# Kernel tuning notes

Hardware: AMD Instinct MI355X
Metric: run time of the kernel (lower is better)

## Reference

```python
import math
import jax, jax.numpy as jnp
import numpy as np

B, S, D, H = 4, 2048, 1024, 16
HD = D // H
EPS = 1e-5
NEG = 1e10


def setup_inputs() -> dict:
    key = jax.random.key(0)
    ks = jax.random.split(key, 6)
    std = 0.02
    return {
        "x": jax.random.normal(ks[0], (B, S, D), dtype=jnp.float32),
        "ln1_w": jnp.ones((D,), jnp.float32),
        "ln1_b": jnp.zeros((D,), jnp.float32),
        "W_attn": jax.random.normal(ks[1], (D, 3 * D), jnp.float32) * std,
        "b_attn": jnp.zeros((3 * D,), jnp.float32),
        "W_cproj": jax.random.normal(ks[2], (D, D), jnp.float32) * std,
        "b_cproj": jnp.zeros((D,), jnp.float32),
        "ln2_w": jnp.ones((D,), jnp.float32),
        "ln2_b": jnp.zeros((D,), jnp.float32),
        "W_fc": jax.random.normal(ks[3], (D, 4 * D), jnp.float32) * std,
        "b_fc": jnp.zeros((4 * D,), jnp.float32),
        "W_mproj": jax.random.normal(ks[4], (4 * D, D), jnp.float32) * std,
        "b_mproj": jnp.zeros((D,), jnp.float32),
    }


def _layernorm(x, w, b):
    u = jnp.mean(x, axis=-1, keepdims=True)
    s = jnp.mean((x - u) ** 2, axis=-1, keepdims=True)
    return w * ((x - u) / jnp.sqrt(s + EPS)) + b


def _gelu(x):
    return 0.5 * x * (1 + jnp.tanh(math.sqrt(2 / math.pi) * (x + 0.044715 * x ** 3)))


def _block(x, ln1_w, ln1_b, W_attn, b_attn, W_cproj, b_cproj,
           ln2_w, ln2_b, W_fc, b_fc, W_mproj, b_mproj):
    h = _layernorm(x, ln1_w, ln1_b)
    qkv = h @ W_attn + b_attn                       # [B,S,3D]
    q, k, v = jnp.split(qkv, 3, axis=-1)
    # split heads -> [B,H,S,hd]
    q = q.reshape(B, S, H, HD).transpose(0, 2, 1, 3)
    k = k.reshape(B, S, H, HD).transpose(0, 2, 1, 3)
    v = v.reshape(B, S, H, HD).transpose(0, 2, 1, 3)
    w = jnp.einsum('bhqd,bhkd->bhqk', q, k) / math.sqrt(HD)
    bias = jnp.tril(jnp.ones((S, S), jnp.float32))  # causal mask
    w = w * bias - NEG * (1 - bias)
    w = jax.nn.softmax(w, axis=-1)
    a = jnp.einsum('bhqk,bhkd->bhqd', w, v)
    a = a.transpose(0, 2, 1, 3).reshape(B, S, D)    # merge heads
    a = a @ W_cproj + b_cproj
    x = x + a                                        # residual
    m = _layernorm(x, ln2_w, ln2_b)
    m = _gelu(m @ W_fc + b_fc) @ W_mproj + b_mproj
    return x + m


def reference(x, ln1_w, ln1_b, W_attn, b_attn, W_cproj, b_cproj,
              ln2_w, ln2_b, W_fc, b_fc, W_mproj, b_mproj):
    return _block(x, ln1_w, ln1_b, W_attn, b_attn, W_cproj, b_cproj,
                  ln2_w, ln2_b, W_fc, b_fc, W_mproj, b_mproj)
```

## Files before the change

### kernel.cpp

```cpp
#include <hip/hip_runtime.h>
#include <hip/hip_bf16.h>
#include <math.h>


typedef __attribute__((ext_vector_type(8))) short short8;
typedef __attribute__((ext_vector_type(4))) float floatx4;
typedef __attribute__((ext_vector_type(2))) unsigned int uint2v;

#define MFMA16(a, b, c) __builtin_amdgcn_mfma_f32_16x16x32_bf16((a), (b), (c), 0, 0, 0)

__device__ __forceinline__ short f2bf(float f) {
    union { float f; unsigned u; } a; a.f = f;
    unsigned r = a.u + 0x7fffu + ((a.u >> 16) & 1u);
    return (short)(r >> 16);
}

__device__ __forceinline__ float bf2f(unsigned short u) {
    union { unsigned u; float f; } a; a.u = ((unsigned)u) << 16;
    return a.f;
}

__device__ __forceinline__ float fast_rcp(float x) {
#if defined(__HIP_DEVICE_COMPILE__)
    return __builtin_amdgcn_rcpf(x);
#else
    return 1.0f / x;
#endif
}

__device__ __forceinline__ float gelu_f(float x) {
    const float u = x + 0.044715f * x * x * x;
    const float t = exp2f(2.302118131f * u);
    return x - x * fast_rcp(t + 1.0f);
}

__device__ __forceinline__ void gload_lds16(const short* g, short* l) {
    __builtin_amdgcn_global_load_lds((const __attribute__((address_space(1))) void*)g,
                                     (__attribute__((address_space(3))) void*)l, 16, 0, 0);
}

__device__ __forceinline__ void tcast_body(const float* __restrict__ W,
                                           short* __restrict__ Wt,
                                           int K, int N, int bxi, int byi,
                                           float* __restrict__ tile) {
    const int t = threadIdx.x;
    const int tx = t & 31;
    const int ty = t >> 5;
    const int bx = bxi * 32;
    const int by = byi * 32;
#pragma unroll
    for (int i = 0; i < 32; i += 8)
        tile[(ty + i) * 33 + tx] = W[(size_t)(by + ty + i) * N + bx + tx];
    __syncthreads();
#pragma unroll
    for (int i = 0; i < 32; i += 8)
        Wt[(size_t)(bx + ty + i) * K + by + tx] = f2bf(tile[tx * 33 + ty + i]);
}

__global__ __launch_bounds__(256) void prep_kernel(
    const float* __restrict__ x, const float* __restrict__ ln_w,
    const float* __restrict__ ln_b, short* __restrict__ hout,
    const float* __restrict__ W_attn, short* __restrict__ W1t,
    const float* __restrict__ W_cproj, short* __restrict__ W2t,
    const float* __restrict__ W_fc, short* __restrict__ W3t,
    const float* __restrict__ W_mproj, short* __restrict__ W4t) {
    __shared__ float smem_f[32 * 33];
    int bid = blockIdx.x;
    if (bid < 8192) {
        const int row = bid;
        const int t = threadIdx.x;
        const float4 v = ((const float4*)(x + (size_t)row * 1024))[t];
        float s = v.x + v.y + v.z + v.w;
        float s2 = v.x * v.x + v.y * v.y + v.z * v.z + v.w * v.w;
#pragma unroll
        for (int d = 32; d >= 1; d >>= 1) {
            s += __shfl_xor(s, d, 64);
            s2 += __shfl_xor(s2, d, 64);
        }
        float* red = smem_f;
        const int wid = t >> 6, lane = t & 63;
        if (lane == 0) { red[wid * 2] = s; red[wid * 2 + 1] = s2; }
        __syncthreads();
        s = red[0] + red[2] + red[4] + red[6];
        s2 = red[1] + red[3] + red[5] + red[7];
        const float mean = s * (1.f / 1024.f);
        const float var = s2 * (1.f / 1024.f) - mean * mean;
        const float rstd = rsqrtf(var + 1e-5f);
        const float4 wv = ((const float4*)ln_w)[t];
        const float4 bv = ((const float4*)ln_b)[t];
        union { ushort4 u; short sa[4]; } ov;
        ov.sa[0] = f2bf(wv.x * ((v.x - mean) * rstd) + bv.x);
        ov.sa[1] = f2bf(wv.y * ((v.y - mean) * rstd) + bv.y);
        ov.sa[2] = f2bf(wv.z * ((v.z - mean) * rstd) + bv.z);
        ov.sa[3] = f2bf(wv.w * ((v.w - mean) * rstd) + bv.w);
        ((ushort4*)(hout + (size_t)row * 1024))[t] = ov.u;
        return;
    }
    bid -= 8192;
    if (bid < 3072) {
        tcast_body(W_attn, W1t, 1024, 3072, bid % 96, bid / 96, smem_f);
        return;
    }
    bid -= 3072;
    if (bid < 1024) {
        tcast_body(W_cproj, W2t, 1024, 1024, bid % 32, bid / 32, smem_f);
        return;
    }
    bid -= 1024;
    if (bid < 4096) {
        tcast_body(W_fc, W3t, 1024, 4096, bid % 128, bid / 128, smem_f);
        return;
    }
    bid -= 4096;
    tcast_body(W_mproj, W4t, 4096, 1024, bid % 32, bid / 32, smem_f);
}

__global__ __launch_bounds__(256) void reduce_kernel(
    const unsigned short* __restrict__ p0, const unsigned short* __restrict__ p1,
    const float* __restrict__ bias, const float* __restrict__ res,
    float* __restrict__ out) {
    const int row = blockIdx.x;
    const int t = threadIdx.x;
    const size_t off = (size_t)row * 1024;
    const ushort4 a = ((const ushort4*)(p0 + off))[t];
    const ushort4 c = ((const ushort4*)(p1 + off))[t];
    const float4 r = ((const float4*)(res + off))[t];
    const float4 bv = ((const float4*)bias)[t];
    float4 o;
    o.x = bf2f(a.x) + bf2f(c.x) + bv.x + r.x;
    o.y = bf2f(a.y) + bf2f(c.y) + bv.y + r.y;
    o.z = bf2f(a.z) + bf2f(c.z) + bv.z + r.z;
    o.w = bf2f(a.w) + bf2f(c.w) + bv.w + r.w;
    ((float4*)(out + off))[t] = o;
}

__global__ __launch_bounds__(256) void reduce_ln_kernel(
    const unsigned short* __restrict__ p0, const unsigned short* __restrict__ p1,
    const float* __restrict__ bias, const float* __restrict__ res,
    float* __restrict__ x2out,
    const float* __restrict__ w, const float* __restrict__ b,
    short* __restrict__ hout) {
    const int row = blockIdx.x;
    const int t = threadIdx.x;
    const size_t off = (size_t)row * 1024;
    const ushort4 a = ((const ushort4*)(p0 + off))[t];
    const ushort4 c = ((const ushort4*)(p1 + off))[t];
    const float4 r = ((const float4*)(res + off))[t];
    const float4 bv = ((const float4*)bias)[t];
    float4 v;
    v.x = bf2f(a.x) + bf2f(c.x) + bv.x + r.x;
    v.y = bf2f(a.y) + bf2f(c.y) + bv.y + r.y;
    v.z = bf2f(a.z) + bf2f(c.z) + bv.z + r.z;
    v.w = bf2f(a.w) + bf2f(c.w) + bv.w + r.w;
    ((float4*)(x2out + off))[t] = v;
    float s = v.x + v.y + v.z + v.w;
    float s2 = v.x * v.x + v.y * v.y + v.z * v.z + v.w * v.w;
#pragma unroll
    for (int d = 32; d >= 1; d >>= 1) {
        s += __shfl_xor(s, d, 64);
        s2 += __shfl_xor(s2, d, 64);
    }
    __shared__ float red[8];
    const int wid = t >> 6, lane = t & 63;
    if (lane == 0) { red[wid * 2] = s; red[wid * 2 + 1] = s2; }
    __syncthreads();
    s = red[0] + red[2] + red[4] + red[6];
    s2 = red[1] + red[3] + red[5] + red[7];
    const float mean = s * (1.f / 1024.f);
    const float var = s2 * (1.f / 1024.f) - mean * mean;
    const float rstd = rsqrtf(var + 1e-5f);
    const float4 wv = ((const float4*)w)[t];
    const float4 lb = ((const float4*)b)[t];
    union { ushort4 u; short sa[4]; } ov;
    ov.sa[0] = f2bf(wv.x * ((v.x - mean) * rstd) + lb.x);
    ov.sa[1] = f2bf(wv.y * ((v.y - mean) * rstd) + lb.y);
    ov.sa[2] = f2bf(wv.z * ((v.z - mean) * rstd) + lb.z);
    ov.sa[3] = f2bf(wv.w * ((v.w - mean) * rstd) + lb.w);
    ((ushort4*)(hout + (size_t)row * 1024))[t] = ov.u;
}

#define GBAR()  asm volatile("s_barrier" ::: "memory")
#define LGKM0() asm volatile("s_waitcnt lgkmcnt(0)" ::: "memory")
#define STAGE_A(b_, kt_, p_)                                                   \
    do {                                                                       \
        gload_lds16(gA + (size_t)((p_) * 128) * lda + (kt_) * 64,              \
                    lA + (b_) * 16384 + (p_) * 8192);                          \
        gload_lds16(gA + (size_t)((p_) * 128 + 64) * lda + (kt_) * 64,         \
                    lA + (b_) * 16384 + (p_) * 8192 + 4096);                   \
    } while (0)
#define STAGE_B(b_, kt_, p_)                                                   \
    do {                                                                       \
        gload_lds16(gB + (size_t)((p_) * 128) * ldb + (kt_) * 64,              \
                    lB + (b_) * 16384 + (p_) * 8192);                          \
        gload_lds16(gB + (size_t)((p_) * 128 + 64) * ldb + (kt_) * 64,         \
                    lB + (b_) * 16384 + (p_) * 8192 + 4096);                   \
    } while (0)

template <int EPI>
__global__ __launch_bounds__(512, 2) void gemm256_kernel(
    const short* __restrict__ A, const short* __restrict__ Bt,
    const float* __restrict__ bias,
    void* __restrict__ Cout, int M, int N, int Klen, int lda, int ldb) {
    extern __shared__ __align__(16) short lds[];
    short* As = lds;
    short* Bs = lds + 32768;

    const int tid = threadIdx.x;
    const int wid = tid >> 6;
    const int lane = tid & 63;
    const int quad = lane >> 4;
    const int l16 = lane & 15;
    const int l7 = l16 & 7;
    const int warp_m = wid >> 2;
    const int warp_n = wid & 3;

    const unsigned gx = gridDim.x;
    const unsigned bid2 = blockIdx.x + gx * blockIdx.y;
    const unsigned xcd = bid2 & 7;
    const unsigned loc = bid2 >> 3;
    const unsigned nb = loc % gx;
    const unsigned mhi = loc / gx;
    const int m0 = (int)(mhi * 8 + xcd) * 256;
    const int n0 = (int)nb * 256;
    const int kbase = blockIdx.z * Klen;
    const int NT = Klen >> 6;

    const int rsub = tid >> 3;
    const int scol = ((tid & 7) ^ (rsub & 7)) << 3;
    const short* gA = A + (size_t)(m0 + rsub) * lda + kbase + scol;
    const short* gB = Bt + (size_t)(n0 + rsub) * ldb + kbase + scol;
    short* lA = As + wid * 512;
    short* lB = Bs + wid * 512;

    const int sk0 = ((0 | quad) ^ l7) << 3;
    const int sk1 = ((4 | quad) ^ l7) << 3;

    floatx4 acc[8][4] = {};
    short8 afrag[4][2], bA[2][2], bB[2][2];

    STAGE_A(0, 0, 0); STAGE_A(0, 0, 1);
    STAGE_B(0, 0, 0); STAGE_B(0, 0, 1);
    if (NT > 1) {
        STAGE_A(1, 1, 0);
        asm volatile("s_waitcnt vmcnt(2)" ::: "memory");
    } else {
        asm volatile("s_waitcnt vmcnt(0)" ::: "memory");
    }
    GBAR();

    for (int t = 0; t < NT; ++t) {
        const int b = t & 1;
        const int bn = b ^ 1;
        const short* Ab = As + b * 16384 + (warp_m * 128 + l16) * 64;
        const short* Bb = Bs + b * 16384 + (warp_n * 64 + l16) * 64;
#pragma unroll
        for (int mi = 0; mi < 4; mi++) {
            afrag[mi][0] = *(const short8*)(Ab + mi * 1024 + sk0);
            afrag[mi][1] = *(const short8*)(Ab + mi * 1024 + sk1);
        }
#pragma unroll
        for (int ni = 0; ni < 2; ni++) {
            bA[ni][0] = *(const short8*)(Bb + ni * 1024 + sk0);
            bA[ni][1] = *(const short8*)(Bb + ni * 1024 + sk1);
        }
        if (t + 1 < NT) STAGE_A(bn, t + 1, 1);
        GBAR(); LGKM0();
        __builtin_amdgcn_s_setprio(1);
#pragma unroll
        for (int mi = 0; mi < 4; mi++)
#pragma unroll
            for (int ni = 0; ni < 2; ni++) {
                acc[mi][ni] = MFMA16(afrag[mi][0], bA[ni][0], acc[mi][ni]);
                acc[mi][ni] = MFMA16(afrag[mi][1], bA[ni][1], acc[mi][ni]);
            }
        __builtin_amdgcn_s_setprio(0);
        GBAR();
#pragma unroll
        for (int ni = 0; ni < 2; ni++) {
            bB[ni][0] = *(const short8*)(Bb + (2 + ni) * 1024 + sk0);
            bB[ni][1] = *(const short8*)(Bb + (2 + ni) * 1024 + sk1);
        }
        if (t + 1 < NT) STAGE_B(bn, t + 1, 0);
        GBAR(); LGKM0();
        __builtin_amdgcn_s_setprio(1);
#pragma unroll
        for (int mi = 0; mi < 4; mi++)
#pragma unroll
            for (int ni = 0; ni < 2; ni++) {
                acc[mi][2 + ni] = MFMA16(afrag[mi][0], bB[ni][0], acc[mi][2 + ni]);
                acc[mi][2 + ni] = MFMA16(afrag[mi][1], bB[ni][1], acc[mi][2 + ni]);
            }
        __builtin_amdgcn_s_setprio(0);
        GBAR();
#pragma unroll
        for (int mi = 0; mi < 4; mi++) {
            afrag[mi][0] = *(const short8*)(Ab + (4 + mi) * 1024 + sk0);
            afrag[mi][1] = *(const short8*)(Ab + (4 + mi) * 1024 + sk1);
        }
        if (t + 1 < NT) STAGE_B(bn, t + 1, 1);
        GBAR(); LGKM0();
        __builtin_amdgcn_s_setprio(1);
#pragma unroll
        for (int mi = 0; mi < 4; mi++)
#pragma unroll
            for (int ni = 0; ni < 2; ni++) {
                acc[4 + mi][2 + ni] = MFMA16(afrag[mi][0], bB[ni][0], acc[4 + mi][2 + ni]);
                acc[4 + mi][2 + ni] = MFMA16(afrag[mi][1], bB[ni][1], acc[4 + mi][2 + ni]);
            }
        __builtin_amdgcn_s_setprio(0);
        GBAR();
        if (t + 2 < NT) STAGE_A(b, t + 2, 0);
        GBAR();
        __builtin_amdgcn_s_setprio(1);
#pragma unroll
        for (int mi = 0; mi < 4; mi++)
#pragma unroll
            for (int ni = 0; ni < 2; ni++) {
                acc[4 + mi][ni] = MFMA16(afrag[mi][0], bA[ni][0], acc[4 + mi][ni]);
                acc[4 + mi][ni] = MFMA16(afrag[mi][1], bA[ni][1], acc[4 + mi][ni]);
            }
        __builtin_amdgcn_s_setprio(0);
        if (t + 2 < NT) asm volatile("s_waitcnt vmcnt(2)" ::: "memory");
        else            asm volatile("s_waitcnt vmcnt(0)" ::: "memory");
        GBAR();
    }

    float bv4[4] = {0.f, 0.f, 0.f, 0.f};
    if constexpr (EPI != 3) {
#pragma unroll
        for (int ni = 0; ni < 4; ni++)
            bv4[ni] = bias[n0 + warp_n * 64 + ni * 16 + l16];
    }
#pragma unroll
    for (int mi = 0; mi < 8; mi++) {
#pragma unroll
        for (int r = 0; r < 4; r++) {
            const int row = m0 + warp_m * 128 + mi * 16 + quad * 4 + r;
            const size_t rowoff = (size_t)row * N + n0 + warp_n * 64 + l16;
#pragma unroll
            for (int ni = 0; ni < 4; ni++) {
                const size_t idx = rowoff + ni * 16;
                float v = acc[mi][ni][r] + bv4[ni];
                if constexpr (EPI == 0) {
                    ((short*)Cout)[idx] = f2bf(v);
                } else if constexpr (EPI == 1) {
                    ((short*)Cout)[idx] = f2bf(gelu_f(v));
                } else {
                    ((short*)Cout)[(size_t)blockIdx.z * M * N + idx] = f2bf(v);
                }
            }
        }
    }
}
#undef STAGE_A
#undef STAGE_B
#undef GBAR
#undef LGKM0

__global__ __launch_bounds__(256) void attn_kernel(
    const short* __restrict__ qkv, short* __restrict__ aout,
    short* __restrict__ O0buf, float* __restrict__ m0p, float* __restrict__ l0p,
    float* __restrict__ m1p, float* __restrict__ l1p) {
    __shared__ __align__(16) short smem[18432];
    short* Ks = smem;
    short* Vt = smem + 64 * 72;

    const int tid = threadIdx.x;
    const int wid = tid >> 6;
    const int lane = tid & 63;
    const int quad = lane >> 4;
    const int l16 = lane & 15;

    const int y = blockIdx.y;
    int qt, ktlo, kthi, mode;
    if (y < 8)       { qt = 8 + y;        ktlo = 0;  kthi = 16;             mode = 1; }
    else if (y < 16) { qt = 15 - y;       ktlo = 0;  kthi = (qt + 1) * 2;   mode = 0; }
    else             { qt = 8 + (23 - y); ktlo = 16; kthi = (qt + 1) * 2;   mode = 2; }
    const int q0 = qt * 128;
    const int bh = blockIdx.x;
    const int b = bh >> 4;
    const int h = bh & 15;

    const short* base = qkv + (size_t)b * 2048 * 3072 + h * 64;
    const int qrow_base = q0 + wid * 32;

    short8 qf[2][2];
#pragma unroll
    for (int qt_i = 0; qt_i < 2; qt_i++)
#pragma unroll
        for (int ks = 0; ks < 2; ks++)
            qf[qt_i][ks] = *(const short8*)(base +
                (size_t)(qrow_base + qt_i * 16 + l16) * 3072 + ks * 32 + quad * 8);

    const int kr_ = tid >> 2;
    const int kcg = (tid & 3) * 16;
    const short* ksrc = base + 1024 + kcg;
    short* kdst = &Ks[kr_ * 72 + kcg];
    const int vrA = ((lane >> 3) << 2) | ((lane >> 1) & 3);
    const short* vsrc = base + 2048 + wid * 16 + (lane & 1) * 8;
    short* vdst = Vt + wid * 1024 + lane * 8;

    const unsigned vaddr0 =
        (unsigned)(size_t)(__attribute__((address_space(3))) void*)Vt +
        (unsigned)(quad * 128 + l16 * 8);

    union VF { short8 s; uint2v h2[2]; };
    union PK { short8 s; unsigned u[4]; };

    floatx4 o[4][2] = {};
    float mrow[2] = {-1e30f, -1e30f};
    float lrow[2] = {0.f, 0.f};
    const float SCL = 0.125f * 1.44269504f;

    uint4 krg0, krg1, vrg0, vrg1;
#define LOADREG(kt0_)                                                          \
    do {                                                                       \
        const short* kp = ksrc + (size_t)((kt0_) + kr_) * 3072;                \
        krg0 = ((const uint4*)kp)[0];                                          \
        krg1 = ((const uint4*)kp)[1];                                          \
        vrg0 = *(const uint4*)(vsrc + (size_t)((kt0_) + vrA) * 3072);          \
        vrg1 = *(const uint4*)(vsrc + (size_t)((kt0_) + vrA + 32) * 3072);     \
    } while (0)

    LOADREG(ktlo * 64);
    for (int kt = ktlo; kt < kthi; kt++) {
        const int kt0 = kt * 64;
        const int bo = (kt & 1) * 9216;
        *(uint4*)(kdst + bo) = krg0;
        *(uint4*)(kdst + bo + 8) = krg1;
        *(uint4*)(vdst + bo) = vrg0;
        *(uint4*)(vdst + bo + 512) = vrg1;
        if (kt + 1 < kthi) LOADREG((kt + 1) * 64);
        __syncthreads();
        if (kt0 <= qrow_base + 31) {
            floatx4 st[4][2] = {};
            __builtin_amdgcn_s_setprio(1);
#pragma unroll
            for (int kti = 0; kti < 4; kti++) {
                const short8 kf0 = *(const short8*)&Ks[bo + (kti * 16 + l16) * 72 + quad * 8];
                const short8 kf1 = *(const short8*)&Ks[bo + (kti * 16 + l16) * 72 + 32 + quad * 8];
#pragma unroll
                for (int qt_i = 0; qt_i < 2; qt_i++) {
                    st[kti][qt_i] = MFMA16(kf0, qf[qt_i][0], st[kti][qt_i]);
                    st[kti][qt_i] = MFMA16(kf1, qf[qt_i][1], st[kti][qt_i]);
                }
            }
            __builtin_amdgcn_s_setprio(0);
            const unsigned va = vaddr0 + (unsigned)(bo * 2);
            VF vf[2][4];
#define TRRD(dst, offs) \
    asm volatile("ds_read_b64_tr_b16 %0, %1 offset:" offs : "=v"(dst) : "v"(va))
            TRRD(vf[0][0].h2[0], "0");    TRRD(vf[0][0].h2[1], "512");
            TRRD(vf[0][1].h2[0], "2048"); TRRD(vf[0][1].h2[1], "2560");
            TRRD(vf[0][2].h2[0], "4096"); TRRD(vf[0][2].h2[1], "4608");
            TRRD(vf[0][3].h2[0], "6144"); TRRD(vf[0][3].h2[1], "6656");
            TRRD(vf[1][0].h2[0], "1024"); TRRD(vf[1][0].h2[1], "1536");
            TRRD(vf[1][1].h2[0], "3072"); TRRD(vf[1][1].h2[1], "3584");
            TRRD(vf[1][2].h2[0], "5120"); TRRD(vf[1][2].h2[1], "5632");
            TRRD(vf[1][3].h2[0], "7168"); TRRD(vf[1][3].h2[1], "7680");
#undef TRRD
            const bool needmask = (kt0 + 63) > qrow_base;
            PK pk[2][2];
#pragma unroll
            for (int qt_i = 0; qt_i < 2; qt_i++) {
                const int q = qrow_base + qt_i * 16 + l16;
                if (needmask) {
#pragma unroll
                    for (int kti = 0; kti < 4; kti++)
#pragma unroll
                        for (int r = 0; r < 4; r++)
                            if ((kt0 + kti * 16 + quad * 4 + r) > q) st[kti][qt_i][r] = -1e30f;
                }
                float mk[4];
#pragma unroll
                for (int kti = 0; kti < 4; kti++)
                    mk[kti] = fmaxf(fmaxf(st[kti][qt_i][0], st[kti][qt_i][1]),
                                    fmaxf(st[kti][qt_i][2], st[kti][qt_i][3]));
                float mx = fmaxf(fmaxf(mk[0], mk[1]), fmaxf(mk[2], mk[3]));
                mx = fmaxf(mx, __shfl_xor(mx, 16, 64));
                mx = fmaxf(mx, __shfl_xor(mx, 32, 64));
                if (!__all((mx - mrow[qt_i]) <= 8.0f)) {
                    const float mnew = fmaxf(mrow[qt_i], mx);
                    const float alpha = exp2f((mrow[qt_i] - mnew) * SCL);
                    mrow[qt_i] = mnew;
                    lrow[qt_i] *= alpha;
#pragma unroll
                    for (int dt = 0; dt < 4; dt++) o[dt][qt_i] *= alpha;
                }
                const float nm = -mrow[qt_i] * SCL;
#pragma unroll
                for (int kti = 0; kti < 4; kti++)
#pragma unroll
                    for (int r = 0; r < 4; r++)
                        st[kti][qt_i][r] = exp2f(fmaf(st[kti][qt_i][r], SCL, nm));
                float sk_[4];
#pragma unroll
                for (int kti = 0; kti < 4; kti++)
                    sk_[kti] = (st[kti][qt_i][0] + st[kti][qt_i][1]) +
                               (st[kti][qt_i][2] + st[kti][qt_i][3]);
                float ps = (sk_[0] + sk_[1]) + (sk_[2] + sk_[3]);
                ps += __shfl_xor(ps, 16, 64);
                ps += __shfl_xor(ps, 32, 64);
                lrow[qt_i] += ps;
#define CVTPK(dst, lo, hi) \
    asm("v_cvt_pk_bf16_f32 %0, %1, %2" : "=v"(dst) : "v"(lo), "v"(hi))
                CVTPK(pk[0][qt_i].u[0], st[0][qt_i][0], st[0][qt_i][1]);
                CVTPK(pk[0][qt_i].u[1], st[0][qt_i][2], st[0][qt_i][3]);
                CVTPK(pk[0][qt_i].u[2], st[1][qt_i][0], st[1][qt_i][1]);
                CVTPK(pk[0][qt_i].u[3], st[1][qt_i][2], st[1][qt_i][3]);
                CVTPK(pk[1][qt_i].u[0], st[2][qt_i][0], st[2][qt_i][1]);
                CVTPK(pk[1][qt_i].u[1], st[2][qt_i][2], st[2][qt_i][3]);
                CVTPK(pk[1][qt_i].u[2], st[3][qt_i][0], st[3][qt_i][1]);
                CVTPK(pk[1][qt_i].u[3], st[3][qt_i][2], st[3][qt_i][3]);
#undef CVTPK
            }
            asm volatile("s_waitcnt lgkmcnt(0)" ::: "memory");
            __builtin_amdgcn_sched_barrier(0);
            __builtin_amdgcn_s_setprio(1);
#pragma unroll
            for (int c = 0; c < 2; c++)
#pragma unroll
                for (int dt = 0; dt < 4; dt++) {
                    o[dt][0] = MFMA16(vf[c][dt].s, pk[c][0].s, o[dt][0]);
                    o[dt][1] = MFMA16(vf[c][dt].s, pk[c][1].s, o[dt][1]);
                }
            __builtin_amdgcn_s_setprio(0);
        }
    }
#undef LOADREG
    __syncthreads();
    const int slot = (qt - 8) * 64 + bh;
    short* Ow = smem + wid * (32 * 72);
    const float rl0 = (mode == 0) ? fast_rcp(lrow[0]) : 1.0f;
    const float rl1 = (mode == 0) ? fast_rcp(lrow[1]) : 1.0f;
#pragma unroll
    for (int dt = 0; dt < 4; dt++)
#pragma unroll
        for (int r = 0; r < 4; r++) {
            Ow[(l16) * 72 + dt * 16 + quad * 4 + r] = f2bf(o[dt][0][r] * rl0);
            Ow[(16 + l16) * 72 + dt * 16 + quad * 4 + r] = f2bf(o[dt][1][r] * rl1);
        }
    if (mode != 0 && quad == 0) {
        const int qi0 = slot * 128 + (qrow_base - q0) + l16;
        if (mode == 1) {
            m0p[qi0] = mrow[0]; l0p[qi0] = lrow[0];
            m0p[qi0 + 16] = mrow[1]; l0p[qi0 + 16] = lrow[1];
        } else {
            m1p[qi0] = mrow[0]; l1p[qi0] = lrow[0];
            m1p[qi0 + 16] = mrow[1]; l1p[qi0 + 16] = lrow[1];
        }
    }
    __asm__ volatile("s_waitcnt lgkmcnt(0)" ::: "memory");
    {
        const int ql = lane >> 1;
        const int h2 = lane & 1;
        short* orow;
        if (mode == 1)
            orow = O0buf + (size_t)slot * 8192 + (size_t)(wid * 32 + ql) * 64 + h2 * 32;
        else
            orow = aout + (size_t)(b * 2048 + q0 + wid * 32 + ql) * 1024 + h * 64 + h2 * 32;
#pragma unroll
        for (int s = 0; s < 4; s++)
            *(uint4*)(orow + s * 8) = *(const uint4*)&Ow[ql * 72 + h2 * 32 + s * 8];
    }
}

__global__ __launch_bounds__(256) void attn_combine_kernel(
    const short* __restrict__ O0buf, short* __restrict__ aout,
    const float* __restrict__ m0p, const float* __restrict__ l0p,
    const float* __restrict__ m1p, const float* __restrict__ l1p) {
    const int slot = blockIdx.x;
    const int qt = 8 + (slot >> 6);
    const int bh = slot & 63;
    const int b = bh >> 4;
    const int h = bh & 15;
    const int t = threadIdx.x;
    const float SCL = 0.125f * 1.44269504f;
#pragma unroll
    for (int rep = 0; rep < 2; rep++) {
        const int ql = rep * 64 + (t >> 2);
        const int dg = (t & 3) * 16;
        const int qi = slot * 128 + ql;
        const float m0 = m0p[qi], l0 = l0p[qi], m1 = m1p[qi], l1 = l1p[qi];
        const float mm = fmaxf(m0, m1);
        const float w0 = exp2f((m0 - mm) * SCL);
        const float w1 = exp2f((m1 - mm) * SCL);
        const float rl = fast_rcp(fmaf(l0, w0, l1 * w1));
        const float f0 = w0 * rl, f1 = w1 * rl;
        const short* p0 = O0buf + (size_t)slot * 8192 + (size_t)ql * 64 + dg;
        short* pout = aout + (size_t)(b * 2048 + qt * 128 + ql) * 1024 + h * 64 + dg;
        union { uint4 v; unsigned short u[8]; } a0, a1, ov;
#pragma unroll
        for (int half = 0; half < 2; half++) {
            a0.v = ((const uint4*)p0)[half];
            a1.v = ((const uint4*)pout)[half];
#pragma unroll
            for (int j = 0; j < 8; j++)
                ov.u[j] = (unsigned short)f2bf(bf2f(a0.u[j]) * f0 + bf2f(a1.u[j]) * f1);
            ((uint4*)pout)[half] = ov.v;
        }
    }
}

extern "C" void kernel_launch(void* const* d_in, const int* in_sizes, int n_in,
                              void* d_out, int out_size, void* d_ws, size_t ws_size,
                              hipStream_t stream) {
    const float* x       = (const float*)d_in[0];
    const float* ln1_w   = (const float*)d_in[1];
    const float* ln1_b   = (const float*)d_in[2];
    const float* W_attn  = (const float*)d_in[3];
    const float* b_attn  = (const float*)d_in[4];
    const float* W_cproj = (const float*)d_in[5];
    const float* b_cproj = (const float*)d_in[6];
    const float* ln2_w   = (const float*)d_in[7];
    const float* ln2_b   = (const float*)d_in[8];
    const float* W_fc    = (const float*)d_in[9];
    const float* b_fc    = (const float*)d_in[10];
    const float* W_mproj = (const float*)d_in[11];
    const float* b_mproj = (const float*)d_in[12];

    char* ws = (char*)d_ws;
    short* W1t  = (short*)(ws + 0);
    short* W2t  = (short*)(ws + 6291456);
    short* W3t  = (short*)(ws + 8388608);
    short* W4t  = (short*)(ws + 16777216);
    short* h    = (short*)(ws + 25165824);
    short* aout = (short*)(ws + 41943040);
    short* big  = (short*)(ws + 58720256);
    short* O0buf = h;
    float* m0p = (float*)(ws + 25165824 + 8388608);
    float* l0p = (float*)(ws + 25165824 + 8388608 + 262144);
    float* m1p = (float*)(ws + 25165824 + 8388608 + 524288);
    float* l1p = (float*)(ws + 25165824 + 8388608 + 786432);
    short* pbuf = h;
    float* x2   = (float*)d_out;
    float* out  = (float*)d_out;

    hipLaunchKernelGGL(prep_kernel, dim3(20480), dim3(256), 0, stream,
                       x, ln1_w, ln1_b, h,
                       W_attn, W1t, W_cproj, W2t, W_fc, W3t, W_mproj, W4t);

    hipLaunchKernelGGL((gemm256_kernel<0>), dim3(12, 32, 1), dim3(512), 131072, stream,
                       h, W1t, b_attn, (void*)big,
                       8192, 3072, 1024, 1024, 1024);

    hipLaunchKernelGGL(attn_kernel, dim3(64, 24), dim3(256), 0, stream,
                       big, aout, O0buf, m0p, l0p, m1p, l1p);
    hipLaunchKernelGGL(attn_combine_kernel, dim3(512), dim3(256), 0, stream,
                       O0buf, aout, m0p, l0p, m1p, l1p);

    hipLaunchKernelGGL((gemm256_kernel<3>), dim3(4, 32, 2), dim3(512), 131072, stream,
                       aout, W2t, (const float*)nullptr, (void*)big,
                       8192, 1024, 512, 1024, 1024);
    hipLaunchKernelGGL(reduce_ln_kernel, dim3(8192), dim3(256), 0, stream,
                       (const unsigned short*)big,
                       (const unsigned short*)(big + (size_t)8192 * 1024),
                       b_cproj, x, x2, ln2_w, ln2_b, h);

    hipLaunchKernelGGL((gemm256_kernel<1>), dim3(16, 32, 1), dim3(512), 131072, stream,
                       h, W3t, b_fc, (void*)big,
                       8192, 4096, 1024, 1024, 1024);

    hipLaunchKernelGGL((gemm256_kernel<3>), dim3(4, 32, 2), dim3(512), 131072, stream,
                       big, W4t, (const float*)nullptr, (void*)pbuf,
                       8192, 1024, 2048, 4096, 4096);
    hipLaunchKernelGGL(reduce_kernel, dim3(8192), dim3(256), 0, stream,
                       (const unsigned short*)pbuf,
                       (const unsigned short*)(pbuf + (size_t)8192 * 1024),
                       b_mproj, x2, out);
}
```

Measured before the change: 491.4 us.

## Split causal attention KV ranges finer for better load balance across blocks

Reworks the attention work split from 24 to 32 row-blocks per head. Long query tiles are now split into two or three KV chunks and medium tiles into two. Partial outputs and their max/sum statistics go to extra scratch buffers placed in the output tensor, and the combine kernel merges up to three partials. The goal is to even out per-block work under the causal mask and reduce tail imbalance. The cost is more partial writes and reads plus a larger combine kernel.

```diff
diff --git a/kernel.cpp b/kernel.cpp
--- a/kernel.cpp
+++ b/kernel.cpp
@@ -360,10 +360,19 @@
 __global__ __launch_bounds__(256) void attn_kernel(
     const short* __restrict__ qkv, short* __restrict__ aout,
     short* __restrict__ O0buf, float* __restrict__ m0p, float* __restrict__ l0p,
-    float* __restrict__ m1p, float* __restrict__ l1p) {
+    float* __restrict__ m1p, float* __restrict__ l1p, char* __restrict__ scratch) {
     __shared__ __align__(16) short smem[18432];
     short* Ks = smem;
     short* Vt = smem + 64 * 72;
+
+    short* O2buf = (short*)scratch;
+    short* O3buf = (short*)(scratch + 4194304);
+    float* m2p = (float*)(scratch + 8388608);
+    float* l2p = (float*)(scratch + 8519680);
+    float* m3p = (float*)(scratch + 8650752);
+    float* l3p = (float*)(scratch + 8781824);
+    float* m4p = (float*)(scratch + 8912896);
+    float* l4p = (float*)(scratch + 9043968);
 
     const int tid = threadIdx.x;
     const int wid = tid >> 6;
@@ -373,9 +382,12 @@
 
     const int y = blockIdx.y;
     int qt, ktlo, kthi, mode;
-    if (y < 8)       { qt = 8 + y;        ktlo = 0;  kthi = 16;             mode = 1; }
-    else if (y < 16) { qt = 15 - y;       ktlo = 0;  kthi = (qt + 1) * 2;   mode = 0; }
-    else             { qt = 8 + (23 - y); ktlo = 16; kthi = (qt + 1) * 2;   mode = 2; }
+    if (y < 8)       { qt = 8 + y;        ktlo = 0;       kthi = 12;                      mode = 1; }
+    else if (y < 16) { qt = 8 + (y - 8);  ktlo = 12;      kthi = min(24, (qt + 1) * 2);   mode = 2; }
+    else if (y < 20) { qt = 12 + (y - 16);ktlo = 24;      kthi = (qt + 1) * 2;            mode = 3; }
+    else if (y < 24) { qt = y - 20;       ktlo = 0;       kthi = (qt + 1) * 2;            mode = 0; }
+    else if (y < 28) { qt = 4 + (y - 24); ktlo = 0;       kthi = qt + 1;                  mode = 4; }
+    else             { qt = 4 + (y - 28); ktlo = qt + 1;  kthi = (qt + 1) * 2;            mode = 5; }
     const int q0 = qt * 128;
     const int bh = blockIdx.x;
     const int b = bh >> 4;
@@ -529,7 +541,17 @@
     }
 #undef LOADREG
     __syncthreads();
-    const int slot = (qt - 8) * 64 + bh;
+    int slot = 0;
+    short* Opart = nullptr;
+    float* mp = nullptr; float* lp = nullptr;
+    switch (mode) {
+        case 1: slot = (qt - 8) * 64 + bh;  Opart = O0buf; mp = m0p; lp = l0p; break;
+        case 2: slot = (qt - 8) * 64 + bh;  mp = m1p; lp = l1p; break;
+        case 3: slot = (qt - 12) * 64 + bh; Opart = O2buf; mp = m2p; lp = l2p; break;
+        case 4: slot = (qt - 4) * 64 + bh;  Opart = O3buf; mp = m3p; lp = l3p; break;
+        case 5: slot = (qt - 4) * 64 + bh;  mp = m4p; lp = l4p; break;
+        default: break;
+    }
     short* Ow = smem + wid * (32 * 72);
     const float rl0 = (mode == 0) ? fast_rcp(lrow[0]) : 1.0f;
     const float rl1 = (mode == 0) ? fast_rcp(lrow[1]) : 1.0f;
@@ -542,21 +564,16 @@
         }
     if (mode != 0 && quad == 0) {
         const int qi0 = slot * 128 + (qrow_base - q0) + l16;
-        if (mode == 1) {
-            m0p[qi0] = mrow[0]; l0p[qi0] = lrow[0];
-            m0p[qi0 + 16] = mrow[1]; l0p[qi0 + 16] = lrow[1];
-        } else {
-            m1p[qi0] = mrow[0]; l1p[qi0] = lrow[0];
-            m1p[qi0 + 16] = mrow[1]; l1p[qi0 + 16] = lrow[1];
-        }
+        mp[qi0] = mrow[0]; lp[qi0] = lrow[0];
+        mp[qi0 + 16] = mrow[1]; lp[qi0 + 16] = lrow[1];
     }
     __asm__ volatile("s_waitcnt lgkmcnt(0)" ::: "memory");
     {
         const int ql = lane >> 1;
         const int h2 = lane & 1;
         short* orow;
-        if (mode == 1)
-            orow = O0buf + (size_t)slot * 8192 + (size_t)(wid * 32 + ql) * 64 + h2 * 32;
+        if (Opart)
+            orow = Opart + (size_t)slot * 8192 + (size_t)(wid * 32 + ql) * 64 + h2 * 32;
         else
             orow = aout + (size_t)(b * 2048 + q0 + wid * 32 + ql) * 1024 + h * 64 + h2 * 32;
 #pragma unroll
@@ -568,10 +585,33 @@
 __global__ __launch_bounds__(256) void attn_combine_kernel(
     const short* __restrict__ O0buf, short* __restrict__ aout,
     const float* __restrict__ m0p, const float* __restrict__ l0p,
-    const float* __restrict__ m1p, const float* __restrict__ l1p) {
-    const int slot = blockIdx.x;
-    const int qt = 8 + (slot >> 6);
-    const int bh = slot & 63;
+    const float* __restrict__ m1p, const float* __restrict__ l1p,
+    const char* __restrict__ scratch) {
+    const short* O2buf = (const short*)scratch;
+    const short* O3buf = (const short*)(scratch + 4194304);
+    const float* m2p = (const float*)(scratch + 8388608);
+    const float* l2p = (const float*)(scratch + 8519680);
+    const float* m3p = (const float*)(scratch + 8650752);
+    const float* l3p = (const float*)(scratch + 8781824);
+    const float* m4p = (const float*)(scratch + 8912896);
+    const float* l4p = (const float*)(scratch + 9043968);
+
+    const int s = blockIdx.x;
+    int qt, bh, sA, sC = 0;
+    const short* PA; const float *MA, *LA, *MB, *LB;
+    const short* PC = nullptr; const float *MC = nullptr, *LC = nullptr;
+    if (s < 512) {
+        qt = 8 + (s >> 6); bh = s & 63; sA = s;
+        PA = O0buf + (size_t)s * 8192; MA = m0p; LA = l0p; MB = m1p; LB = l1p;
+        if (qt >= 12) {
+            sC = (qt - 12) * 64 + bh;
+            PC = O2buf + (size_t)sC * 8192; MC = m2p; LC = l2p;
+        }
+    } else {
+        const int s3 = s - 512;
+        qt = 4 + (s3 >> 6); bh = s3 & 63; sA = s3;
+        PA = O3buf + (size_t)s3 * 8192; MA = m3p; LA = l3p; MB = m4p; LB = l4p;
+    }
     const int b = bh >> 4;
     const int h = bh & 15;
     const int t = threadIdx.x;
@@ -580,23 +620,31 @@
     for (int rep = 0; rep < 2; rep++) {
         const int ql = rep * 64 + (t >> 2);
         const int dg = (t & 3) * 16;
-        const int qi = slot * 128 + ql;
-        const float m0 = m0p[qi], l0 = l0p[qi], m1 = m1p[qi], l1 = l1p[qi];
-        const float mm = fmaxf(m0, m1);
+        const int qi = sA * 128 + ql;
+        const float m0 = MA[qi], l0 = LA[qi], m1 = MB[qi], l1 = LB[qi];
+        float mm = fmaxf(m0, m1);
+        float m2v = -1e30f, l2v = 0.f;
+        if (PC) { m2v = MC[sC * 128 + ql]; l2v = LC[sC * 128 + ql]; mm = fmaxf(mm, m2v); }
         const float w0 = exp2f((m0 - mm) * SCL);
         const float w1 = exp2f((m1 - mm) * SCL);
-        const float rl = fast_rcp(fmaf(l0, w0, l1 * w1));
-        const float f0 = w0 * rl, f1 = w1 * rl;
-        const short* p0 = O0buf + (size_t)slot * 8192 + (size_t)ql * 64 + dg;
+        const float w2 = PC ? exp2f((m2v - mm) * SCL) : 0.f;
+        const float rl = fast_rcp(l0 * w0 + l1 * w1 + l2v * w2);
+        const float f0 = w0 * rl, f1 = w1 * rl, f2 = w2 * rl;
+        const short* pA = PA + (size_t)ql * 64 + dg;
+        const short* pC = PC ? PC + (size_t)ql * 64 + dg : nullptr;
         short* pout = aout + (size_t)(b * 2048 + qt * 128 + ql) * 1024 + h * 64 + dg;
-        union { uint4 v; unsigned short u[8]; } a0, a1, ov;
+        union { uint4 v; unsigned short u[8]; } a0, a1, a2, ov;
 #pragma unroll
         for (int half = 0; half < 2; half++) {
-            a0.v = ((const uint4*)p0)[half];
+            a0.v = ((const uint4*)pA)[half];
             a1.v = ((const uint4*)pout)[half];
-#pragma unroll
-            for (int j = 0; j < 8; j++)
-                ov.u[j] = (unsigned short)f2bf(bf2f(a0.u[j]) * f0 + bf2f(a1.u[j]) * f1);
+            if (pC) a2.v = ((const uint4*)pC)[half];
+#pragma unroll
+            for (int j = 0; j < 8; j++) {
+                float acc = bf2f(a0.u[j]) * f0 + bf2f(a1.u[j]) * f1;
+                if (pC) acc += bf2f(a2.u[j]) * f2;
+                ov.u[j] = (unsigned short)f2bf(acc);
+            }
             ((uint4*)pout)[half] = ov.v;
         }
     }
@@ -635,6 +683,7 @@
     short* pbuf = h;
     float* x2   = (float*)d_out;
     float* out  = (float*)d_out;
+    char* scr   = (char*)d_out;
 
     hipLaunchKernelGGL(prep_kernel, dim3(20480), dim3(256), 0, stream,
                        x, ln1_w, ln1_b, h,
@@ -644,10 +693,10 @@
                        h, W1t, b_attn, (void*)big,
                        8192, 3072, 1024, 1024, 1024);
 
-    hipLaunchKernelGGL(attn_kernel, dim3(64, 24), dim3(256), 0, stream,
-                       big, aout, O0buf, m0p, l0p, m1p, l1p);
-    hipLaunchKernelGGL(attn_combine_kernel, dim3(512), dim3(256), 0, stream,
-                       O0buf, aout, m0p, l0p, m1p, l1p);
+    hipLaunchKernelGGL(attn_kernel, dim3(64, 32), dim3(256), 0, stream,
+                       big, aout, O0buf, m0p, l0p, m1p, l1p, scr);
+    hipLaunchKernelGGL(attn_combine_kernel, dim3(768), dim3(256), 0, stream,
+                       O0buf, aout, m0p, l0p, m1p, l1p, (const char*)scr);
 
     hipLaunchKernelGGL((gemm256_kernel<3>), dim3(4, 32, 2), dim3(512), 131072, stream,
                        aout, W2t, (const float*)nullptr, (void*)big,
```

New measurement: 500.6 us. About the same (+1.9%).
